# Optimization experiments

Measured on AMD Instinct MI355X. Metric: run time of the kernel, lower is better.

Reference implementation:

```python
import jax, jax.numpy as jnp
import numpy as np

NUM_NODES = 256
IN_FEAT = 64
HIDDEN = 512
N_CLASSES = 2
BATCH = 256


def setup_inputs() -> dict:
    key = jax.random.key(0)
    ks = jax.random.split(key, 10)
    return {
        "z": jax.random.normal(ks[0], (BATCH, 1, NUM_NODES, NUM_NODES), dtype=jnp.float32),
        "node_emb": jax.random.normal(ks[1], (NUM_NODES, IN_FEAT), dtype=jnp.float32),
        "w1": jax.random.normal(ks[2], (IN_FEAT, HIDDEN), dtype=jnp.float32) * (1.0 / np.sqrt(IN_FEAT)),
        "b1": jnp.zeros((HIDDEN,), dtype=jnp.float32),
        "w2": jax.random.normal(ks[3], (HIDDEN, HIDDEN), dtype=jnp.float32) * (1.0 / np.sqrt(HIDDEN)),
        "b2": jnp.zeros((HIDDEN,), dtype=jnp.float32),
        "w3": jax.random.normal(ks[4], (HIDDEN, HIDDEN), dtype=jnp.float32) * (1.0 / np.sqrt(HIDDEN)),
        "b3": jnp.zeros((HIDDEN,), dtype=jnp.float32),
        "fcw": jax.random.normal(ks[5], (HIDDEN, N_CLASSES), dtype=jnp.float32) * (1.0 / np.sqrt(HIDDEN)),
        "fcb": jnp.zeros((N_CLASSES,), dtype=jnp.float32),
    }


def reference(z, node_emb, w1, b1, w2, b2, w3, b3, fcw, fcb):
    # z: (B, 1, N, N) latent interpreted as weighted adjacency
    z_sq = jnp.squeeze(z, axis=1)                         # (B, N, N)
    A = jax.nn.sigmoid(z_sq)
    A = (A + jnp.swapaxes(A, 1, 2)) * 0.5                  # symmetrize
    A_hat = A + jnp.eye(A.shape[-1], dtype=A.dtype)[None]  # add self loops
    D_hat = jnp.sum(A_hat, axis=2) + 1e-6                  # (B, N) degrees
    d_inv_sqrt = D_hat ** -0.5
    # norm_A = D^{-1/2} A_hat D^{-1/2} via row/col scaling (same math as diag bmm)
    norm_A = A_hat * d_inv_sqrt[:, :, None] * d_inv_sqrt[:, None, :]

    X = jnp.broadcast_to(node_emb[None], (z.shape[0],) + node_emb.shape)  # (B, N, F)
    H1 = jax.nn.relu(jnp.einsum('bij,bjh->bih', norm_A, X @ w1 + b1))
    H2 = jax.nn.relu(jnp.einsum('bij,bjh->bih', norm_A, H1 @ w2 + b2))
    H3 = jax.nn.relu(jnp.einsum('bij,bjh->bih', norm_A, H2 @ w3 + b3))
    graph_emb = jnp.mean(H3, axis=1)                       # (B, H)
    logits = graph_emb @ fcw + fcb                         # (B, n_classes)
    return logits
```

## Files before the change

kernel.cpp:

```cpp
#include <hip/hip_runtime.h>
#include <stdint.h>

#define B_ 256
#define N_ 256
#define F_ 64
#define H_ 512

typedef _Float16 f16;
typedef _Float16 f16x8 __attribute__((ext_vector_type(8)));
typedef _Float16 f16x4 __attribute__((ext_vector_type(4)));
typedef _Float16 f16x2 __attribute__((ext_vector_type(2)));
typedef float    f32x4 __attribute__((ext_vector_type(4)));

__device__ __forceinline__ float sigmoidf_(float x) {
    return 1.0f / (1.0f + __expf(-x));
}

#define BAR_ACQ(N) do { \
    asm volatile("s_waitcnt vmcnt(" #N ")" ::: "memory"); \
    __builtin_amdgcn_s_barrier(); \
    __builtin_amdgcn_sched_barrier(0); } while (0)
#define BAR_REL() do { \
    __builtin_amdgcn_sched_barrier(0); \
    __builtin_amdgcn_s_barrier(); } while (0)

__global__ __launch_bounds__(512) void k_fsum(const float* __restrict__ z,
                                              f16* __restrict__ nA) {
    __shared__ f16 T[256 * 256];
    __shared__ float cpart[8][256];
    __shared__ float rpart[256][2];
    __shared__ float Dv[256];

    const int b = blockIdx.x;
    const int tid = threadIdx.x, lane = tid & 63, w = tid >> 6;
    const float* zb = z + (size_t)b * (N_ * N_);

    auto swz = [](int i) { return (i & 31) ^ (i >> 5); };

    float colacc[4] = {0.f, 0.f, 0.f, 0.f};
    const int ch = lane >> 1, half = lane & 1;
    for (int r = 0; r < 32; r++) {
        int i = w * 32 + r;
        float4 v = *(const float4*)(zb + (size_t)i * N_ + lane * 4);
        float s0 = sigmoidf_(v.x), s1 = sigmoidf_(v.y),
              s2 = sigmoidf_(v.z), s3 = sigmoidf_(v.w);
        f16x4 sv = { (f16)s0, (f16)s1, (f16)s2, (f16)s3 };
        *(f16x4*)&T[i * 256 + ((ch ^ swz(i)) << 3) + half * 4] = sv;
        colacc[0] += s0; colacc[1] += s1; colacc[2] += s2; colacc[3] += s3;
    }
    #pragma unroll
    for (int k = 0; k < 4; k++) cpart[w][lane * 4 + k] = colacc[k];
    __syncthreads();

    {
        int i = tid >> 1, h = tid & 1;
        float s = 0.f;
        #pragma unroll
        for (int c = 0; c < 16; c++) {
            int cc = h * 16 + c;
            f16x8 v = *(const f16x8*)&T[i * 256 + ((cc ^ swz(i)) << 3)];
            #pragma unroll
            for (int k = 0; k < 8; k++) s += (float)v[k];
        }
        rpart[i][h] = s;
    }
    __syncthreads();

    if (tid < 256) {
        float cs = 0.f;
        #pragma unroll
        for (int ww = 0; ww < 8; ww++) cs += cpart[ww][tid];
        float rs = rpart[tid][0] + rpart[tid][1];
        Dv[tid] = rsqrtf(1.0f + 1e-6f + 0.5f * (rs + cs));
    }
    __syncthreads();

    f16* Ob = nA + (size_t)b * (N_ * N_);
    #pragma unroll
    for (int tt = 0; tt < 2; tt++) {
        int tile = tt * 512 + tid;
        int I = tile >> 5, J = tile & 31;
        f16x8 a[8], bm[8];
        #pragma unroll
        for (int r = 0; r < 8; r++) {
            int ia = I * 8 + r;
            a[r] = *(const f16x8*)&T[ia * 256 + ((J ^ swz(ia)) << 3)];
        }
        #pragma unroll
        for (int r = 0; r < 8; r++) {
            int jb = J * 8 + r;
            bm[r] = *(const f16x8*)&T[jb * 256 + ((I ^ swz(jb)) << 3)];
        }
        float dj[8];
        #pragma unroll
        for (int k = 0; k < 8; k++) dj[k] = Dv[J * 8 + k];
        #pragma unroll
        for (int r = 0; r < 8; r++) {
            float di = Dv[I * 8 + r];
            f16x8 o;
            #pragma unroll
            for (int k = 0; k < 8; k++) {
                float v = 0.5f * ((float)a[r][k] + (float)bm[k][r]);
                if (I * 8 + r == J * 8 + k) v += 1.0f;
                o[k] = (f16)(v * di * dj[k]);
            }
            *(f16x8*)&Ob[(size_t)(I * 8 + r) * N_ + J * 8] = o;
        }
    }
}

__global__ __launch_bounds__(256) void k_prep(const float* __restrict__ ne,
                                              const float* __restrict__ w1,
                                              const float* __restrict__ b1,
                                              const float* __restrict__ w2,
                                              const float* __restrict__ w3,
                                              f16* __restrict__ XW1t,
                                              f16* __restrict__ w2t,
                                              f16* __restrict__ w3t) {
    int bid = blockIdx.x;
    if (bid < 512) {
        int h = bid, node = threadIdx.x;
        float s = b1[h];
        #pragma unroll 8
        for (int k = 0; k < F_; k++) s += ne[node * F_ + k] * w1[k * H_ + h];
        XW1t[h * N_ + node] = (f16)s;
    } else {
        int idx4 = bid - 512;
        int which = idx4 >> 10;
        const float* src = which ? w3 : w2;
        f16* dst = which ? w3t : w2t;
        int idx = (idx4 & 1023) * 256 + threadIdx.x;
        int k = idx >> 9, n = idx & 511;
        dst[n * H_ + k] = (f16)src[k * H_ + n];
    }
}

__global__ __launch_bounds__(1024, 4) void k_gemm2(const f16* __restrict__ nA,
                                                   const f16* __restrict__ XW1t,
                                                   f16* __restrict__ H1) {
    __shared__ f16 Bs[2][16384];
    __shared__ f16 Am[2][8192];

    const int tid = threadIdx.x;
    const int lane = tid & 63, wave = tid >> 6;
    const int ln15 = lane & 15, quad = lane >> 4;
    const int wm = wave >> 2, wn = wave & 3;

    const int lin = blockIdx.x;
    const int xcd = lin & 7, p = lin >> 3;
    const int grp = xcd * 64 + p;
    const int b = grp >> 1, m_t = grp & 1;
    const int m0 = m_t * 128;

    const f16* Ab = nA + (size_t)b * (N_ * N_);
    f16* Hb = H1 + (size_t)b * (N_ * H_);

    const int lr = lane >> 3;
    const int kc = (lane & 7) ^ lr;

    auto stage = [&](int s) {
        int pass = (s >> 2) & 1, kt = s & 3, buf = s & 1;
        #pragma unroll
        for (int c = 0; c < 2; c++) {
            int chunk = wave * 2 + c;
            int row = pass * 256 + chunk * 8 + lr;
            __builtin_amdgcn_global_load_lds(
                (__attribute__((address_space(1))) void*)(XW1t + (size_t)row * 256 + kt * 64 + kc * 8),
                (__attribute__((address_space(3))) void*)(&Bs[buf][chunk * 512]), 16, 0, 0);
        }
        {
            int chunk = wave;
            int row = m0 + chunk * 8 + lr;
            __builtin_amdgcn_global_load_lds(
                (__attribute__((address_space(1))) void*)(Ab + (size_t)row * N_ + kt * 64 + kc * 8),
                (__attribute__((address_space(3))) void*)(&Am[buf][chunk * 512]), 16, 0, 0);
        }
    };

    f32x4 acc[4][2];
    #pragma unroll
    for (int i = 0; i < 4; i++)
        #pragma unroll
        for (int j = 0; j < 2; j++)
            #pragma unroll
            for (int r = 0; r < 4; r++) acc[i][j][r] = 0.0f;

    auto cwrite = [&](int pass) {
        #pragma unroll
        for (int mt = 0; mt < 4; mt++) {
            int h0 = pass * 256 + wm * 64 + mt * 16 + quad * 4;
            #pragma unroll
            for (int nt = 0; nt < 2; nt++) {
                int node = m0 + wn * 32 + nt * 16 + ln15;
                f16x4 v;
                #pragma unroll
                for (int rr = 0; rr < 4; rr++) {
                    float x = acc[mt][nt][rr];
                    v[rr] = (f16)(x > 0.f ? x : 0.f);
                }
                *(f16x4*)&Hb[(size_t)node * H_ + h0] = v;
            }
        }
    };

    stage(0);
    for (int s = 0; s < 8; ++s) {
        const int buf = s & 1;
        if (s < 7) {
            stage(s + 1);
            BAR_ACQ(3);
        } else {
            BAR_ACQ(0);
        }
        __builtin_amdgcn_s_setprio(1);
        #pragma unroll
        for (int ks = 0; ks < 2; ks++) {
            const int rkc = ks * 4 + quad;
            f16x8 aF[4], bF[2];
            #pragma unroll
            for (int t = 0; t < 4; t++) {
                int ra = wm * 64 + t * 16 + ln15;
                aF[t] = *(const f16x8*)&Bs[buf][(ra * 8 + (rkc ^ (ra & 7))) * 8];
            }
            #pragma unroll
            for (int t = 0; t < 2; t++) {
                int rb = wn * 32 + t * 16 + ln15;
                bF[t] = *(const f16x8*)&Am[buf][(rb * 8 + (rkc ^ (rb & 7))) * 8];
            }
            #pragma unroll
            for (int mt = 0; mt < 4; mt++)
                #pragma unroll
                for (int nt = 0; nt < 2; nt++)
                    acc[mt][nt] = __builtin_amdgcn_mfma_f32_16x16x32_f16(aF[mt], bF[nt], acc[mt][nt], 0, 0, 0);
        }
        __builtin_amdgcn_s_setprio(0);
        if (s == 3) {
            cwrite(0);
            #pragma unroll
            for (int i = 0; i < 4; i++)
                #pragma unroll
                for (int j = 0; j < 2; j++)
                    #pragma unroll
                    for (int r = 0; r < 4; r++) acc[i][j][r] = 0.0f;
        }
        BAR_REL();
    }
    cwrite(1);
}

template <int REDUCE>
__global__ __launch_bounds__(1024, 4) void k_fused(const f16* __restrict__ Hin,
                                                   const f16* __restrict__ Wt,
                                                   const float* __restrict__ bias,
                                                   const f16* __restrict__ nA,
                                                   f16* __restrict__ Hout,
                                                   float* __restrict__ gp) {
    __shared__ f16 As[2][16384];
    __shared__ f16 WU[32768];

    const int tid  = threadIdx.x;
    const int lane = tid & 63, wave = tid >> 6;
    const int ln15 = lane & 15, quad = lane >> 4;
    const int wm = wave >> 2, wn = wave & 3;

    const int lin = blockIdx.x;
    const int xcd = lin & 7, p = lin >> 3;
    const int grp = xcd * 128 + p;
    const int b = grp >> 2, hc = grp & 3;

    const f16* Hb = Hin + (size_t)b * (N_ * H_);
    const f16* Ab = nA + (size_t)b * (N_ * N_);
    const f16* Wc = Wt + (size_t)(hc * 128) * H_;

    const int lr = lane >> 3;
    const int kc = (lane & 7) ^ lr;

    auto stage1 = [&](int buf, int kt) {
        #pragma unroll
        for (int c = 0; c < 2; c++) {
            int chunk = wave * 2 + c;
            int row = chunk * 8 + lr;
            __builtin_amdgcn_global_load_lds(
                (__attribute__((address_space(1))) void*)(Hb + (size_t)row * H_ + kt * 64 + kc * 8),
                (__attribute__((address_space(3))) void*)(&As[buf][chunk * 512]), 16, 0, 0);
        }
        {
            int chunk = wave;
            int row = chunk * 8 + lr;
            __builtin_amdgcn_global_load_lds(
                (__attribute__((address_space(1))) void*)(Wc + (size_t)row * H_ + kt * 64 + kc * 8),
                (__attribute__((address_space(3))) void*)(&WU[buf * 8192 + chunk * 512]), 16, 0, 0);
        }
    };
    auto stage2 = [&](int buf, int jt) {
        #pragma unroll
        for (int c = 0; c < 2; c++) {
            int chunk = wave * 2 + c;
            int row = chunk * 8 + lr;
            __builtin_amdgcn_global_load_lds(
                (__attribute__((address_space(1))) void*)(Ab + (size_t)row * N_ + jt * 64 + kc * 8),
                (__attribute__((address_space(3))) void*)(&As[buf][chunk * 512]), 16, 0, 0);
        }
    };

    f32x4 acc[4][2];
    #pragma unroll
    for (int i = 0; i < 4; i++)
        #pragma unroll
        for (int j = 0; j < 2; j++)
            #pragma unroll
            for (int r = 0; r < 4; r++) acc[i][j][r] = 0.0f;

    stage1(0, 0);
    for (int kt = 0; kt < 8; ++kt) {
        const int buf = kt & 1;
        if (kt < 7) {
            stage1(buf ^ 1, kt + 1);
            BAR_ACQ(3);
        } else {
            stage2(0, 0);
            BAR_ACQ(2);
        }
        __builtin_amdgcn_s_setprio(1);
        #pragma unroll
        for (int ks = 0; ks < 2; ks++) {
            const int rkc = ks * 4 + quad;
            f16x8 aF[4], bF[2];
            #pragma unroll
            for (int t = 0; t < 4; t++) {
                int ra = wm * 64 + t * 16 + ln15;
                aF[t] = *(const f16x8*)&As[buf][(ra * 8 + (rkc ^ (ra & 7))) * 8];
            }
            #pragma unroll
            for (int t = 0; t < 2; t++) {
                int rb = wn * 32 + t * 16 + ln15;
                bF[t] = *(const f16x8*)&WU[buf * 8192 + (rb * 8 + (rkc ^ (rb & 7))) * 8];
            }
            #pragma unroll
            for (int mt = 0; mt < 4; mt++)
                #pragma unroll
                for (int nt = 0; nt < 2; nt++)
                    acc[mt][nt] = __builtin_amdgcn_mfma_f32_16x16x32_f16(aF[mt], bF[nt], acc[mt][nt], 0, 0, 0);
        }
        __builtin_amdgcn_s_setprio(0);
        BAR_REL();
    }

    #pragma unroll
    for (int nt = 0; nt < 2; nt++) {
        int hl = wn * 32 + nt * 16 + ln15;
        float bv = bias[hc * 128 + hl];
        #pragma unroll
        for (int mt = 0; mt < 4; mt++) {
            int j = wm * 64 + mt * 16 + quad * 4;
            int slot = (j >> 3) ^ (hl & 7);
            f16x4 v;
            #pragma unroll
            for (int rr = 0; rr < 4; rr++) v[rr] = (f16)(acc[mt][nt][rr] + bv);
            *(f16x4*)&WU[hl * 256 + slot * 8 + (j & 7)] = v;
        }
    }
    asm volatile("s_waitcnt lgkmcnt(0)" ::: "memory");
    __builtin_amdgcn_s_barrier();
    __builtin_amdgcn_sched_barrier(0);

    #pragma unroll
    for (int i = 0; i < 4; i++)
        #pragma unroll
        for (int j = 0; j < 2; j++)
            #pragma unroll
            for (int r = 0; r < 4; r++) acc[i][j][r] = 0.0f;

    for (int jt = 0; jt < 4; ++jt) {
        const int buf = jt & 1;
        if (jt < 3) {
            stage2(buf ^ 1, jt + 1);
            BAR_ACQ(2);
        } else {
            BAR_ACQ(0);
        }
        __builtin_amdgcn_s_setprio(1);
        #pragma unroll
        for (int ks = 0; ks < 2; ks++) {
            const int rkc = ks * 4 + quad;
            f16x8 aF[4], bF[2];
            #pragma unroll
            for (int t = 0; t < 4; t++) {
                int ra = wm * 64 + t * 16 + ln15;
                aF[t] = *(const f16x8*)&As[buf][(ra * 8 + (rkc ^ (ra & 7))) * 8];
            }
            #pragma unroll
            for (int t = 0; t < 2; t++) {
                int rb = wn * 32 + t * 16 + ln15;
                int g = jt * 8 + rkc;
                bF[t] = *(const f16x8*)&WU[rb * 256 + ((g ^ (rb & 7)) * 8)];
            }
            #pragma unroll
            for (int mt = 0; mt < 4; mt++)
                #pragma unroll
                for (int nt = 0; nt < 2; nt++)
                    acc[mt][nt] = __builtin_amdgcn_mfma_f32_16x16x32_f16(aF[mt], bF[nt], acc[mt][nt], 0, 0, 0);
        }
        __builtin_amdgcn_s_setprio(0);
        BAR_REL();
    }

    if (REDUCE == 0) {
        f16* Ob = Hout + (size_t)b * (N_ * H_);
        #pragma unroll
        for (int mt = 0; mt < 4; mt++) {
            int node = wm * 64 + mt * 16 + quad * 4;
            #pragma unroll
            for (int nt = 0; nt < 2; nt++) {
                int hg = hc * 128 + wn * 32 + nt * 16 + ln15;
                #pragma unroll
                for (int rr = 0; rr < 4; rr++) {
                    float v = acc[mt][nt][rr];
                    v = v > 0.f ? v : 0.f;
                    Ob[(size_t)(node + rr) * H_ + hg] = (f16)v;
                }
            }
        }
    } else {
        float part[2];
        #pragma unroll
        for (int nt = 0; nt < 2; nt++) {
            float s = 0.f;
            #pragma unroll
            for (int mt = 0; mt < 4; mt++)
                #pragma unroll
                for (int rr = 0; rr < 4; rr++) {
                    float v = acc[mt][nt][rr];
                    s += (v > 0.f ? v : 0.f);
                }
            s += __shfl_down(s, 32, 64);
            s += __shfl_down(s, 16, 64);
            part[nt] = s;
        }
        __syncthreads();
        float* red = (float*)&As[0][0];
        if (quad == 0) {
            #pragma unroll
            for (int nt = 0; nt < 2; nt++)
                red[wave * 32 + nt * 16 + ln15] = part[nt];
        }
        __syncthreads();
        if (tid < 128) {
            int wnl = tid >> 5, cl = tid & 31;
            float g = red[(0 * 4 + wnl) * 32 + cl] + red[(1 * 4 + wnl) * 32 + cl]
                    + red[(2 * 4 + wnl) * 32 + cl] + red[(3 * 4 + wnl) * 32 + cl];
            gp[(size_t)b * H_ + hc * 128 + tid] = g;
        }
    }
}

__global__ __launch_bounds__(256) void k_logits(const float* __restrict__ gp,
                                                const float* __restrict__ fcw,
                                                const float* __restrict__ fcb,
                                                float* __restrict__ out) {
    int b = blockIdx.x, tid = threadIdx.x;
    const float* g = gp + (size_t)b * H_;
    float g0 = g[tid];
    float g1 = g[tid + 256];
    float p0 = g0 * fcw[tid * 2 + 0] + g1 * fcw[(tid + 256) * 2 + 0];
    float p1 = g0 * fcw[tid * 2 + 1] + g1 * fcw[(tid + 256) * 2 + 1];
    for (int off = 32; off; off >>= 1) {
        p0 += __shfl_down(p0, off, 64);
        p1 += __shfl_down(p1, off, 64);
    }
    __shared__ float r0[4], r1[4];
    int lane = tid & 63, w = tid >> 6;
    if (lane == 0) { r0[w] = p0; r1[w] = p1; }
    __syncthreads();
    const float inv = 1.0f / N_;
    if (tid == 0) out[b * 2 + 0] = (r0[0] + r0[1] + r0[2] + r0[3]) * inv + fcb[0];
    if (tid == 1) out[b * 2 + 1] = (r1[0] + r1[1] + r1[2] + r1[3]) * inv + fcb[1];
}

extern "C" void kernel_launch(void* const* d_in, const int* in_sizes, int n_in,
                              void* d_out, int out_size, void* d_ws, size_t ws_size,
                              hipStream_t stream) {
    const float* z   = (const float*)d_in[0];
    const float* ne  = (const float*)d_in[1];
    const float* w1  = (const float*)d_in[2];
    const float* b1  = (const float*)d_in[3];
    const float* w2  = (const float*)d_in[4];
    const float* b2  = (const float*)d_in[5];
    const float* w3  = (const float*)d_in[6];
    const float* b3  = (const float*)d_in[7];
    const float* fcw = (const float*)d_in[8];
    const float* fcb = (const float*)d_in[9];
    float* out = (float*)d_out;

    char* ws = (char*)d_ws;
    f16*   T     = (f16*)(ws + 0);
    f16*   nA    = (f16*)(ws + 67108864);
    f16*   Hh    = (f16*)(ws + 100663296);
    float* gpart = (float*)(ws + 100663296);
    f16*   XW1t  = (f16*)(ws + 167772160);
    f16*   w2t   = (f16*)(ws + 168034304);
    f16*   w3t   = (f16*)(ws + 168558592);

    k_fsum<<<256, 512, 0, stream>>>(z, nA);
    k_prep<<<2560, 256, 0, stream>>>(ne, w1, b1, w2, w3, XW1t, w2t, w3t);

    k_gemm2<<<512, 1024, 0, stream>>>(nA, XW1t, Hh);
    k_fused<0><<<1024, 1024, 0, stream>>>(Hh, w2t, b2, nA, T, nullptr);
    k_fused<1><<<1024, 1024, 0, stream>>>(T, w3t, b3, nA, nullptr, gpart);

    k_logits<<<B_, 256, 0, stream>>>(gpart, fcw, fcb, out);
}
```

Measured before the change: 301.9 us.

## Merge adjacency normalization and weight prep into one front kernel

Combines the sigmoid/symmetrize/normalize kernel and the weight-prep kernel into a single 1024-thread launch whose blocks branch by index. The adjacency path uses 16 waves with fewer rows per wave, and the XW1 and weight-transpose paths now stage data through LDS for coalesced loads and stores instead of strided global accesses. This removes a launch and lets the small prep work overlap the z pass. The cost is heavier register and LDS pressure per block in the adjacency path, which could lower occupancy.

```diff
diff --git a/kernel.cpp b/kernel.cpp
--- a/kernel.cpp
+++ b/kernel.cpp
@@ -24,68 +24,69 @@
     __builtin_amdgcn_sched_barrier(0); \
     __builtin_amdgcn_s_barrier(); } while (0)
 
-__global__ __launch_bounds__(512) void k_fsum(const float* __restrict__ z,
-                                              f16* __restrict__ nA) {
+__global__ __launch_bounds__(1024, 4) void k_front(const float* __restrict__ z,
+                                                   const float* __restrict__ ne,
+                                                   const float* __restrict__ w1,
+                                                   const float* __restrict__ b1,
+                                                   const float* __restrict__ w2,
+                                                   const float* __restrict__ w3,
+                                                   f16* __restrict__ nA,
+                                                   f16* __restrict__ XW1t,
+                                                   f16* __restrict__ w2t,
+                                                   f16* __restrict__ w3t) {
     __shared__ f16 T[256 * 256];
-    __shared__ float cpart[8][256];
-    __shared__ float rpart[256][2];
+    __shared__ float cpart[16][256];
+    __shared__ float rpart[256][4];
     __shared__ float Dv[256];
 
-    const int b = blockIdx.x;
-    const int tid = threadIdx.x, lane = tid & 63, w = tid >> 6;
-    const float* zb = z + (size_t)b * (N_ * N_);
-
+    const int bid = blockIdx.x, tid = threadIdx.x;
     auto swz = [](int i) { return (i & 31) ^ (i >> 5); };
 
-    float colacc[4] = {0.f, 0.f, 0.f, 0.f};
-    const int ch = lane >> 1, half = lane & 1;
-    for (int r = 0; r < 32; r++) {
-        int i = w * 32 + r;
-        float4 v = *(const float4*)(zb + (size_t)i * N_ + lane * 4);
-        float s0 = sigmoidf_(v.x), s1 = sigmoidf_(v.y),
-              s2 = sigmoidf_(v.z), s3 = sigmoidf_(v.w);
-        f16x4 sv = { (f16)s0, (f16)s1, (f16)s2, (f16)s3 };
-        *(f16x4*)&T[i * 256 + ((ch ^ swz(i)) << 3) + half * 4] = sv;
-        colacc[0] += s0; colacc[1] += s1; colacc[2] += s2; colacc[3] += s3;
-    }
-    #pragma unroll
-    for (int k = 0; k < 4; k++) cpart[w][lane * 4 + k] = colacc[k];
-    __syncthreads();
-
-    {
-        int i = tid >> 1, h = tid & 1;
-        float s = 0.f;
-        #pragma unroll
-        for (int c = 0; c < 16; c++) {
-            int cc = h * 16 + c;
-            f16x8 v = *(const f16x8*)&T[i * 256 + ((cc ^ swz(i)) << 3)];
-            #pragma unroll
-            for (int k = 0; k < 8; k++) s += (float)v[k];
-        }
-        rpart[i][h] = s;
-    }
-    __syncthreads();
-
-    if (tid < 256) {
-        float cs = 0.f;
-        #pragma unroll
-        for (int ww = 0; ww < 8; ww++) cs += cpart[ww][tid];
-        float rs = rpart[tid][0] + rpart[tid][1];
-        Dv[tid] = rsqrtf(1.0f + 1e-6f + 0.5f * (rs + cs));
-    }
-    __syncthreads();
-
-    f16* Ob = nA + (size_t)b * (N_ * N_);
-    #pragma unroll
-    for (int tt = 0; tt < 2; tt++) {
-        int tile = tt * 512 + tid;
-        int I = tile >> 5, J = tile & 31;
-        f16x8 a[8], bm[8];
-        #pragma unroll
-        for (int r = 0; r < 8; r++) {
-            int ia = I * 8 + r;
-            a[r] = *(const f16x8*)&T[ia * 256 + ((J ^ swz(ia)) << 3)];
-        }
+    if (bid < 256) {
+        const int lane = tid & 63, w = tid >> 6;
+        const float* zb = z + (size_t)bid * (N_ * N_);
+
+        float colacc[4] = {0.f, 0.f, 0.f, 0.f};
+        const int ch = lane >> 1, half = lane & 1;
+        for (int r = 0; r < 16; r++) {
+            int i = w * 16 + r;
+            float4 v = *(const float4*)(zb + (size_t)i * N_ + lane * 4);
+            float s0 = sigmoidf_(v.x), s1 = sigmoidf_(v.y),
+                  s2 = sigmoidf_(v.z), s3 = sigmoidf_(v.w);
+            f16x4 sv = { (f16)s0, (f16)s1, (f16)s2, (f16)s3 };
+            *(f16x4*)&T[i * 256 + ((ch ^ swz(i)) << 3) + half * 4] = sv;
+            colacc[0] += s0; colacc[1] += s1; colacc[2] += s2; colacc[3] += s3;
+        }
+        #pragma unroll
+        for (int k = 0; k < 4; k++) cpart[w][lane * 4 + k] = colacc[k];
+        __syncthreads();
+
+        {
+            int i = tid >> 2, q = tid & 3;
+            float s = 0.f;
+            #pragma unroll
+            for (int c = 0; c < 8; c++) {
+                int cc = q * 8 + c;
+                f16x8 v = *(const f16x8*)&T[i * 256 + ((cc ^ swz(i)) << 3)];
+                #pragma unroll
+                for (int k = 0; k < 8; k++) s += (float)v[k];
+            }
+            rpart[i][q] = s;
+        }
+        __syncthreads();
+
+        if (tid < 256) {
+            float cs = 0.f;
+            #pragma unroll
+            for (int ww = 0; ww < 16; ww++) cs += cpart[ww][tid];
+            float rs = rpart[tid][0] + rpart[tid][1] + rpart[tid][2] + rpart[tid][3];
+            Dv[tid] = rsqrtf(1.0f + 1e-6f + 0.5f * (rs + cs));
+        }
+        __syncthreads();
+
+        f16* Ob = nA + (size_t)bid * (N_ * N_);
+        int I = tid >> 5, J = tid & 31;
+        f16x8 bm[8];
         #pragma unroll
         for (int r = 0; r < 8; r++) {
             int jb = J * 8 + r;
@@ -96,42 +97,58 @@
         for (int k = 0; k < 8; k++) dj[k] = Dv[J * 8 + k];
         #pragma unroll
         for (int r = 0; r < 8; r++) {
-            float di = Dv[I * 8 + r];
+            int ia = I * 8 + r;
+            float di = Dv[ia];
+            f16x8 a = *(const f16x8*)&T[ia * 256 + ((J ^ swz(ia)) << 3)];
             f16x8 o;
             #pragma unroll
             for (int k = 0; k < 8; k++) {
-                float v = 0.5f * ((float)a[r][k] + (float)bm[k][r]);
-                if (I * 8 + r == J * 8 + k) v += 1.0f;
+                float v = 0.5f * ((float)a[k] + (float)bm[k][r]);
+                if (ia == J * 8 + k) v += 1.0f;
                 o[k] = (f16)(v * di * dj[k]);
             }
-            *(f16x8*)&Ob[(size_t)(I * 8 + r) * N_ + J * 8] = o;
-        }
-    }
-}
-
-__global__ __launch_bounds__(256) void k_prep(const float* __restrict__ ne,
-                                              const float* __restrict__ w1,
-                                              const float* __restrict__ b1,
-                                              const float* __restrict__ w2,
-                                              const float* __restrict__ w3,
-                                              f16* __restrict__ XW1t,
-                                              f16* __restrict__ w2t,
-                                              f16* __restrict__ w3t) {
-    int bid = blockIdx.x;
-    if (bid < 512) {
-        int h = bid, node = threadIdx.x;
+            *(f16x8*)&Ob[(size_t)ia * N_ + J * 8] = o;
+        }
+    } else if (bid < 384) {
+        float* neL = (float*)T;
+        #pragma unroll
+        for (int it = 0; it < 4; it++) {
+            int idx = it * 1024 + tid;
+            int node = idx >> 4, k4 = idx & 15;
+            float4 v = *(const float4*)(ne + (size_t)node * F_ + k4 * 4);
+            neL[(k4 * 4 + 0) * 256 + node] = v.x;
+            neL[(k4 * 4 + 1) * 256 + node] = v.y;
+            neL[(k4 * 4 + 2) * 256 + node] = v.z;
+            neL[(k4 * 4 + 3) * 256 + node] = v.w;
+        }
+        __syncthreads();
+        int gid = (bid - 256) * 1024 + tid;
+        int h = gid >> 8, node = gid & 255;
         float s = b1[h];
         #pragma unroll 8
-        for (int k = 0; k < F_; k++) s += ne[node * F_ + k] * w1[k * H_ + h];
+        for (int k = 0; k < F_; k++) s += neL[k * 256 + node] * w1[k * H_ + h];
         XW1t[h * N_ + node] = (f16)s;
     } else {
-        int idx4 = bid - 512;
-        int which = idx4 >> 10;
-        const float* src = which ? w3 : w2;
-        f16* dst = which ? w3t : w2t;
-        int idx = (idx4 & 1023) * 256 + threadIdx.x;
-        int k = idx >> 9, n = idx & 511;
-        dst[n * H_ + k] = (f16)src[k * H_ + n];
+        int t = bid - 384;
+        const float* src = (t >= 64) ? w3 : w2;
+        f16* dst = (t >= 64) ? w3t : w2t;
+        t &= 63;
+        const int K0 = (t >> 3) * 64, N0 = (t & 7) * 64;
+        f16* ldsT = T;
+        {
+            int r = tid >> 4, l16 = tid & 15;
+            float4 v = *(const float4*)(src + (size_t)(K0 + r) * H_ + N0 + l16 * 4);
+            ldsT[(l16 * 4 + 0) * 72 + r] = (f16)v.x;
+            ldsT[(l16 * 4 + 1) * 72 + r] = (f16)v.y;
+            ldsT[(l16 * 4 + 2) * 72 + r] = (f16)v.z;
+            ldsT[(l16 * 4 + 3) * 72 + r] = (f16)v.w;
+        }
+        __syncthreads();
+        if (tid < 512) {
+            int n_l = tid >> 3, c8 = tid & 7;
+            f16x8 o = *(const f16x8*)&ldsT[n_l * 72 + c8 * 8];
+            *(f16x8*)&dst[(size_t)(N0 + n_l) * H_ + K0 + c8 * 8] = o;
+        }
     }
 }
 
@@ -501,8 +518,7 @@
     f16*   w2t   = (f16*)(ws + 168034304);
     f16*   w3t   = (f16*)(ws + 168558592);
 
-    k_fsum<<<256, 512, 0, stream>>>(z, nA);
-    k_prep<<<2560, 256, 0, stream>>>(ne, w1, b1, w2, w3, XW1t, w2t, w3t);
+    k_front<<<512, 1024, 0, stream>>>(z, ne, w1, b1, w2, w3, nA, XW1t, w2t, w3t);
 
     k_gemm2<<<512, 1024, 0, stream>>>(nA, XW1t, Hh);
     k_fused<0><<<1024, 1024, 0, stream>>>(Hh, w2t, b2, nA, T, nullptr);
```

Result: faster. 283.3 us (-6.2%).
